# Kernel optimization log

Hardware: AMD Instinct MI355X
Metric: run time of the kernel (lower is better)

Reference implementation:

```python
import jax, jax.numpy as jnp
import numpy as np

B, T, D, H, O, L = 32, 512, 512, 512, 2, 2


def setup_inputs() -> dict:
    key = jax.random.key(0)
    ks = jax.random.split(key, 8)
    s_in = 1.0 / np.sqrt(D + H)
    s_h = 1.0 / np.sqrt(H + H)
    x = jax.random.normal(ks[0], (B, T, D), dtype=jnp.float32)
    # Fused gate weights per layer: columns ordered [forget | input | candidate | output]
    W0 = jax.random.uniform(ks[1], (D + H, 4 * H), jnp.float32, -s_in, s_in)
    b0 = jax.random.uniform(ks[2], (4 * H,), jnp.float32, -s_in, s_in)
    W1 = jax.random.uniform(ks[3], (H + H, 4 * H), jnp.float32, -s_h, s_h)
    b1 = jax.random.uniform(ks[4], (4 * H,), jnp.float32, -s_h, s_h)
    s_r = 1.0 / np.sqrt(H)
    Wr = jax.random.uniform(ks[5], (H, O), jnp.float32, -s_r, s_r)
    br = jax.random.uniform(ks[6], (O,), jnp.float32, -s_r, s_r)
    return {"x": x, "W0": W0, "b0": b0, "W1": W1, "b1": b1, "Wr": Wr, "br": br}


def _lstm_cell(xt, h, c, W, b):
    # One fused GEMM for all 4 gates, then elementwise gate math.
    z = jnp.concatenate([xt, h], axis=1) @ W + b  # [B, 4H]
    f, i, g, o = jnp.split(z, 4, axis=1)
    new_c = c * jax.nn.sigmoid(f) + jnp.tanh(g) * jax.nn.sigmoid(i)
    # NB: original module applies tanh to the OLD cell state c (faithful to source).
    new_h = jax.nn.sigmoid(o) * jnp.tanh(c)
    return new_h, new_c


def reference(x, W0, b0, W1, b1, Wr, br):
    Bb = x.shape[0]
    zeros = jnp.zeros((Bb, H), dtype=x.dtype)

    def step(carry, xt):
        h1, c1, h2, c2 = carry
        nh1, nc1 = _lstm_cell(xt, h1, c1, W0, b0)
        nh2, nc2 = _lstm_cell(nh1, h2, c2, W1, b1)
        return (nh1, nc1, nh2, nc2), nh2

    _, ys = jax.lax.scan(step, (zeros, zeros, zeros, zeros), jnp.swapaxes(x, 0, 1))
    out = jnp.swapaxes(ys, 0, 1)  # [B, T, H]
    return out @ Wr + br  # [B, T, O]
```

## Files before the change

kernel.cpp:

```cpp
#include <hip/hip_runtime.h>
#include <hip/hip_bf16.h>
#include <stdint.h>

typedef unsigned short u16;
typedef unsigned int u32;
typedef unsigned long long u64;
typedef __attribute__((ext_vector_type(8))) short bf16x8;
typedef __attribute__((ext_vector_type(4))) float f32x4;
typedef __attribute__((ext_vector_type(4))) u32 u32x4;

#define TT 512
#define WPS ((size_t)2048 * 1024)
#define ZRS 8
#define HRS 16
#define HRS2 4

#define LD16C(dst, addr) asm volatile("global_load_dwordx4 %0, %1, off sc0 sc1" : "=v"(dst) : "v"(addr))
#define LD8C(dst, addr)  asm volatile("global_load_dwordx2 %0, %1, off sc0 sc1" : "=v"(dst) : "v"(addr))
#define LD4C(dst, addr)  asm volatile("global_load_dword %0, %1, off sc0 sc1"   : "=v"(dst) : "v"(addr))
#define ST4C(addr, v)    asm volatile("global_store_dword %0, %1, off sc0 sc1"  :: "v"(addr), "v"(v) : "memory")
#define ST8C(addr, v)    asm volatile("global_store_dwordx2 %0, %1, off sc0 sc1":: "v"(addr), "v"(v) : "memory")
#define ST16C(addr, v)   asm volatile("global_store_dwordx4 %0, %1, off sc0 sc1":: "v"(addr), "v"(v) : "memory")
#define VM0()            do { asm volatile("s_waitcnt vmcnt(0)" ::: "memory"); \
                              __builtin_amdgcn_sched_barrier(0); } while (0)

__device__ __forceinline__ u16 f2bf(float f) {
  u32 u = __builtin_bit_cast(u32, f);
  return (u16)((u + 0x7FFFu + ((u >> 16) & 1u)) >> 16);
}
__device__ __forceinline__ float bf2f(u16 h) {
  u32 u = ((u32)h) << 16;
  return __builtin_bit_cast(float, u);
}
__device__ __forceinline__ float sigm(float x) { return 1.0f / (1.0f + expf(-x)); }
__device__ __forceinline__ f32x4 mfma16(bf16x8 a, bf16x8 b, f32x4 c) {
  return __builtin_amdgcn_mfma_f32_16x16x32_bf16(a, b, c, 0, 0, 0);
}
__device__ __forceinline__ u32 cvtpk(float a, float b) {
  u32 r;
  asm volatile("v_cvt_pk_bf16_f32 %0, %1, %2" : "=v"(r) : "v"(a), "v"(b));
  return r;
}
__device__ __forceinline__ void mark_err(u32* err) {
  __hip_atomic_fetch_add(err, 1u, __ATOMIC_RELAXED, __HIP_MEMORY_SCOPE_AGENT);
}
__device__ __forceinline__ u64 pack3(float v, u32 tag) {
  u16 p0 = f2bf(v); float r1 = v - bf2f(p0);
  u16 p1 = f2bf(r1); u16 p2 = f2bf(r1 - bf2f(p1));
  return (u64)((u32)p0 | ((u32)p1 << 16)) | ((u64)((u32)p2 | (tag << 16)) << 32);
}
__device__ __forceinline__ float zval(u64 w) {
  return bf2f((u16)(w & 0xFFFFu)) + bf2f((u16)((w >> 16) & 0xFFFFu))
       + bf2f((u16)((w >> 32) & 0xFFFFu));
}

__device__ __forceinline__ void wait_slots(const u32* slots, int ln, u32 tgt,
                                           u32* lastv, int* bail, u32* err) {
  if (*bail) return;
  if (__ballot(*lastv < tgt) == 0ull) return;
  const u32* ptr = slots + (ln & 31);
  int n = 0;
  for (;;) {
    u32 v;
    LD4C(v, ptr);
    VM0();
    if (v > *lastv) *lastv = v;
    if (__ballot(*lastv < tgt) == 0ull) return;
    __builtin_amdgcn_s_sleep(2);
    if (++n > 400000) { *bail = 1; if (ln == 0) mark_err(err); return; }
  }
}

__device__ __forceinline__ void head_poll(const u64* ptr, u32 texp, u32* err) {
  int n = 0;
  for (;;) {
    u64 hw;
    LD8C(hw, ptr);
    VM0();
    if (__ballot((u32)(hw >> 48) != texp) == 0ull) return;
    __builtin_amdgcn_s_sleep(1);
    if (++n > 600000) { if ((threadIdx.x & 63) == 0) mark_err(err); return; }
  }
}

__global__ void prep_w(const float* __restrict__ W, u16* __restrict__ WT) {
  int i = blockIdx.x * 256 + threadIdx.x;
  if (i >= 2048 * 1024) return;
  int n = i >> 10, k = i & 1023;
  float v = W[(size_t)k * 2048 + n];
  u16 p0 = f2bf(v);  float r  = v - bf2f(p0);
  u16 p1 = f2bf(r);  float r2 = r - bf2f(p1);
  u16 p2 = f2bf(r2);
  size_t o = (size_t)n * 1024 + k;
  WT[o] = p0;
  WT[WPS + o] = p1;
  WT[2 * WPS + o] = p2;
}

template <int LAYER>
__device__ void chain(char* smem, int p, int bid,
                      const float* __restrict__ bias,
                      const u16* __restrict__ WT,
                      const u64* Zring, u64* hG,
                      const u32* progOther, u32* progSelf,
                      u16* h2hi, u32* err) {
  u16* wl = (u16*)smem;
  float* zl = (float*)(smem + 131072);
  const int tid = threadIdx.x;

#pragma unroll 1
  for (int it = 0; it < 32; ++it) {
    int id = it * 256 + tid;
    int pl = id >> 12, rem = id & 4095, rho = rem >> 6, m = rem & 63;
    int n = ((rho >> 4) << 9) + (bid << 4) + (rho & 15);
    u32x4 v = *(const u32x4*)(WT + (size_t)pl * WPS + (size_t)n * 1024 + 512 + m * 8);
    int dst = pl * 65536 + rho * 1024 + ((m << 4) ^ ((rho & 7) << 4));
    *(u32x4*)((char*)wl + dst) = v;
  }

  const int ln = tid & 63, kq = tid >> 6;
  const int fr = ln & 15, kg8 = (ln >> 4) << 3;
  const int row = tid >> 4, hc = tid & 15;
  float bsv[4];
#pragma unroll
  for (int g = 0; g < 4; ++g) bsv[g] = bias[(g << 9) + (bid << 4) + hc];
  const int ka = kq * 128 + kg8;
  const u16* w2base[4];
#pragma unroll
  for (int nt = 0; nt < 4; ++nt)
    w2base[nt] = WT + 2 * WPS + (size_t)((nt << 9) + (bid << 4) + fr) * 1024 + 512 + ka;
  const int hrm = (LAYER == 1) ? (HRS - 1) : (HRS2 - 1);
  const int pcol = ((ln >> 1) << 4) + ((ln & 1) << 9);

  float creg = 0.0f;
  u32 lastbp = 0;
  int bail = 0;
  __syncthreads();

#pragma unroll 1
  for (int t = 0; t < TT; ++t) {
    if (LAYER == 1 && kq == 0 && t >= HRS - 1)
      wait_slots(progOther, ln, (u32)(t - (HRS - 1)), &lastbp, &bail, err);

    const size_t soff = (size_t)(t & hrm) * 8192;
    const u64* hb = hG + soff + (size_t)fr * 512 + ka;
    const u64* zb = Zring + (size_t)(t & (ZRS - 1)) * (16 * 2048) + (size_t)row * 2048
                  + (bid << 4) + hc;
    const u32 texp = (u32)t, zexp = (u32)(t + 1);

    u64 zw[4];
#pragma unroll
    for (int g = 0; g < 4; ++g) LD8C(zw[g], zb + ((size_t)g << 9));

    head_poll(hG + soff + pcol, texp, err);

    u32x4 hv[4][4];
    int tries = 0;
    for (;;) {
#pragma unroll
      for (int kt = 0; kt < 4; ++kt)
#pragma unroll
        for (int j = 0; j < 4; ++j) LD16C(hv[kt][j], hb + kt * 32 + 2 * j);
      VM0();
      u32 bad = 0;
#pragma unroll
      for (int kt = 0; kt < 4; ++kt)
#pragma unroll
        for (int j = 0; j < 4; ++j)
          bad |= ((hv[kt][j].y >> 16) ^ texp) | ((hv[kt][j].w >> 16) ^ texp);
      if (__ballot(bad != 0) == 0ull) break;
      if (++tries > 500000) { if (ln == 0) mark_err(err); break; }
      __builtin_amdgcn_s_sleep(1);
    }

    f32x4 acc[4] = {{0.f,0.f,0.f,0.f},{0.f,0.f,0.f,0.f},{0.f,0.f,0.f,0.f},{0.f,0.f,0.f,0.f}};
#pragma unroll
    for (int kt = 0; kt < 4; ++kt) {
      u32 r0[4], r1[4], r2[4];
#pragma unroll
      for (int j = 0; j < 4; ++j) {
        u32 lo0 = hv[kt][j].x, hi0 = hv[kt][j].y, lo1 = hv[kt][j].z, hi1 = hv[kt][j].w;
        r0[j] = (lo0 & 0xFFFFu) | (lo1 << 16);
        r1[j] = (lo0 >> 16) | (lo1 & 0xFFFF0000u);
        r2[j] = (hi0 & 0xFFFFu) | (hi1 << 16);
      }
      bf16x8 a0 = __builtin_bit_cast(bf16x8, *(u32x4*)r0);
      bf16x8 a1 = __builtin_bit_cast(bf16x8, *(u32x4*)r1);
      bf16x8 a2 = __builtin_bit_cast(bf16x8, *(u32x4*)r2);
#pragma unroll
      for (int nt = 0; nt < 4; ++nt) {
        int rho = (nt << 4) + fr;
        int kb = ((ka + kt * 32) << 1) ^ ((rho & 7) << 4);
        bf16x8 w0 = *(const bf16x8*)((char*)wl + rho * 1024 + kb);
        bf16x8 w1 = *(const bf16x8*)((char*)wl + 65536 + rho * 1024 + kb);
        bf16x8 w2 = *(const bf16x8*)(w2base[nt] + kt * 32);
        acc[nt] = mfma16(a0, w0, acc[nt]);
        acc[nt] = mfma16(a1, w0, acc[nt]);
        acc[nt] = mfma16(a2, w0, acc[nt]);
        acc[nt] = mfma16(a0, w1, acc[nt]);
        acc[nt] = mfma16(a1, w1, acc[nt]);
        acc[nt] = mfma16(a0, w2, acc[nt]);
      }
    }
    const int r4 = (ln >> 4) << 2;
    if (kq < 2) {
#pragma unroll
      for (int nt = 0; nt < 4; ++nt)
#pragma unroll
        for (int r = 0; r < 4; ++r)
          zl[(kq * 16 + r4 + r) * 66 + (nt << 4) + fr] = acc[nt][r];
    }
    __syncthreads();
    if (kq >= 2) {
#pragma unroll
      for (int nt = 0; nt < 4; ++nt)
#pragma unroll
        for (int r = 0; r < 4; ++r)
          zl[((kq - 2) * 16 + r4 + r) * 66 + (nt << 4) + fr] += acc[nt][r];
    }
    __syncthreads();

    int ztries = 0;
    for (;;) {
      u32 zbad = 0;
#pragma unroll
      for (int g = 0; g < 4; ++g) zbad |= ((u32)(zw[g] >> 48) ^ zexp);
      if (__ballot(zbad != 0) == 0ull) break;
      __builtin_amdgcn_s_sleep(1);
#pragma unroll
      for (int g = 0; g < 4; ++g) LD8C(zw[g], zb + ((size_t)g << 9));
      VM0();
      if (++ztries > 500000) { if (ln == 0) mark_err(err); break; }
    }
    float z4[4];
#pragma unroll
    for (int g = 0; g < 4; ++g)
      z4[g] = zl[row * 66 + (g << 4) + hc] + zl[(16 + row) * 66 + (g << 4) + hc]
            + zval(zw[g]) + bsv[g];
    float sf = sigm(z4[0]);
    float si = sigm(z4[1]);
    float tg = tanhf(z4[2]);
    float sog = sigm(z4[3]);
    float hn = sog * tanhf(creg);
    creg = creg * sf + tg * si;
    u64 word = pack3(hn, (u32)(t + 1));
    size_t ho = (size_t)((t + 1) & hrm) * 8192 + (size_t)row * 512 + (bid << 4) + hc;
    ST8C(hG + ho, word);
    if (LAYER == 2)
      h2hi[(size_t)(t + 1) * 16384 + (size_t)(p * 16 + row) * 512 + (bid << 4) + hc] =
          (u16)(word & 0xFFFFu);
    __syncthreads();
    if (tid == 0) ST4C(progSelf + bid, (u32)(t + 1));
  }
}

__device__ void worker(char* smem, int w, const float* __restrict__ x,
                       const u16* __restrict__ W0T, const u16* __restrict__ W1T,
                       const u64* h1G, u64* Z0R, u64* ZcR,
                       const u32* prog1, const u32* prog2, u32* err) {
  const int s = w & 63, q = w >> 6;
  u16* wl1 = (u16*)smem;
  u16* wl0 = (u16*)(smem + 65536);
  float* zl = (float*)(smem + 131072);
  const int tid = threadIdx.x;

#pragma unroll 1
  for (int it = 0; it < 32; ++it) {
    int id = it * 256 + tid;
    int sl = id >> 12, rem = id & 4095, pl = rem >> 11, rem2 = rem & 2047;
    int rho = rem2 >> 6, m = rem2 & 63;
    const u16* WT = sl ? W0T : W1T;
    u32x4 v = *(const u32x4*)(WT + (size_t)pl * WPS + (size_t)(32 * s + rho) * 1024 + m * 8);
    int dst = sl * 65536 + pl * 32768 + rho * 1024 + ((m << 4) ^ ((rho & 7) << 4));
    *(u32x4*)((char*)wl1 + dst) = v;
  }

  const int ln = tid & 63, kq = tid >> 6;
  const int fr = ln & 15, kg8 = (ln >> 4) << 3;
  const int row = tid >> 4, c2 = (tid & 15) * 2;
  const int ka = kq * 128 + kg8;
  const int pcol = ((ln >> 1) << 4) + ((ln & 1) << 9);
  u32 last2[2] = {0, 0}, lastbp[2] = {0, 0};
  int bail = 0;
  __syncthreads();

#pragma unroll 1
  for (int k = 0;; ++k) {
    int t = 2 * k + q;
    if (t > 511) break;

    int nz = (k < 3) ? 2 : 1;
#pragma unroll 1
    for (int e = 0; e < nz; ++e) {
      int tz = (e == 0 && k < 3) ? t : t + 6;
      if (tz > 511) continue;
#pragma unroll 1
      for (int p = 0; p < 2; ++p) {
        if (kq == 0 && tz >= ZRS)
          wait_slots(prog1 + p * 32, ln, (u32)(tz - ZRS + 1), &lastbp[p], &bail, err);
        const float* xb = x + (size_t)(p * 16 + fr) * TT * 512 + (size_t)tz * 512 + ka;
        f32x4 acc[2] = {{0.f,0.f,0.f,0.f},{0.f,0.f,0.f,0.f}};
#pragma unroll
        for (int kt = 0; kt < 4; ++kt) {
          f32x4 f0 = *(const f32x4*)(xb + kt * 32);
          f32x4 f1 = *(const f32x4*)(xb + kt * 32 + 4);
          u32 r0[4], r1[4], r2[4];
#pragma unroll
          for (int j = 0; j < 4; ++j) {
            float v0 = (j < 2) ? f0[j * 2] : f1[(j - 2) * 2];
            float v1 = (j < 2) ? f0[j * 2 + 1] : f1[(j - 2) * 2 + 1];
            u32 pk0 = cvtpk(v0, v1);
            float h0 = __builtin_bit_cast(float, pk0 << 16);
            float h1f = __builtin_bit_cast(float, pk0 & 0xFFFF0000u);
            float q0 = v0 - h0, q1 = v1 - h1f;
            u32 pk1 = cvtpk(q0, q1);
            float g0 = __builtin_bit_cast(float, pk1 << 16);
            float g1 = __builtin_bit_cast(float, pk1 & 0xFFFF0000u);
            u32 s0 = __builtin_bit_cast(u32, q0 - g0);
            u32 s1 = __builtin_bit_cast(u32, q1 - g1);
            r0[j] = pk0; r1[j] = pk1;
            r2[j] = (s0 >> 16) | (s1 & 0xFFFF0000u);
          }
          bf16x8 a0 = __builtin_bit_cast(bf16x8, *(u32x4*)r0);
          bf16x8 a1 = __builtin_bit_cast(bf16x8, *(u32x4*)r1);
          bf16x8 a2 = __builtin_bit_cast(bf16x8, *(u32x4*)r2);
#pragma unroll
          for (int nt = 0; nt < 2; ++nt) {
            int rho = (nt << 4) + fr;
            int kb = ((ka + kt * 32) << 1) ^ ((rho & 7) << 4);
            bf16x8 w0 = *(const bf16x8*)((char*)wl0 + rho * 1024 + kb);
            bf16x8 w1 = *(const bf16x8*)((char*)wl0 + 32768 + rho * 1024 + kb);
            bf16x8 w2 = *(const bf16x8*)(W0T + 2 * WPS + (size_t)(32 * s + rho) * 1024 + ka + kt * 32);
            acc[nt] = mfma16(a0, w0, acc[nt]);
            acc[nt] = mfma16(a1, w0, acc[nt]);
            acc[nt] = mfma16(a2, w0, acc[nt]);
            acc[nt] = mfma16(a0, w1, acc[nt]);
            acc[nt] = mfma16(a1, w1, acc[nt]);
            acc[nt] = mfma16(a0, w2, acc[nt]);
          }
        }
        const int r4 = (ln >> 4) << 2;
        if (kq < 2) {
#pragma unroll
          for (int nt = 0; nt < 2; ++nt)
#pragma unroll
            for (int r = 0; r < 4; ++r)
              zl[(kq * 16 + r4 + r) * 34 + (nt << 4) + fr] = acc[nt][r];
        }
        __syncthreads();
        if (kq >= 2) {
#pragma unroll
          for (int nt = 0; nt < 2; ++nt)
#pragma unroll
            for (int r = 0; r < 4; ++r)
              zl[((kq - 2) * 16 + r4 + r) * 34 + (nt << 4) + fr] += acc[nt][r];
        }
        __syncthreads();
        float v0 = zl[row * 34 + c2] + zl[(16 + row) * 34 + c2];
        float v1 = zl[row * 34 + c2 + 1] + zl[(16 + row) * 34 + c2 + 1];
        u64 w0 = pack3(v0, (u32)(tz + 1));
        u64 w1 = pack3(v1, (u32)(tz + 1));
        u32x4 st = { (u32)w0, (u32)(w0 >> 32), (u32)w1, (u32)(w1 >> 32) };
        u64* dst = Z0R + (size_t)p * ZRS * 16 * 2048 + (size_t)(tz & (ZRS - 1)) * (16 * 2048)
                 + (size_t)row * 2048 + 32 * s + c2;
        ST16C(dst, st);
        __syncthreads();
      }
    }

#pragma unroll 1
    for (int p = 0; p < 2; ++p) {
      if (kq == 0 && t >= ZRS)
        wait_slots(prog2 + p * 32, ln, (u32)(t - ZRS + 1), &last2[p], &bail, err);
      const size_t sb = (size_t)p * HRS * 8192 + (size_t)((t + 1) & (HRS - 1)) * 8192;
      const u64* hb = h1G + sb + (size_t)fr * 512 + ka;
      const u32 texp = (u32)(t + 1);
      head_poll(h1G + sb + pcol, texp, err);
      u32x4 hv[4][4];
      int tries = 0;
      for (;;) {
#pragma unroll
        for (int kt = 0; kt < 4; ++kt)
#pragma unroll
          for (int j = 0; j < 4; ++j) LD16C(hv[kt][j], hb + kt * 32 + 2 * j);
        VM0();
        u32 bad = 0;
#pragma unroll
        for (int kt = 0; kt < 4; ++kt)
#pragma unroll
          for (int j = 0; j < 4; ++j)
            bad |= ((hv[kt][j].y >> 16) ^ texp) | ((hv[kt][j].w >> 16) ^ texp);
        if (__ballot(bad != 0) == 0ull) break;
        if (++tries > 500000) { if (ln == 0) mark_err(err); break; }
        __builtin_amdgcn_s_sleep(1);
      }
      f32x4 acc[2] = {{0.f,0.f,0.f,0.f},{0.f,0.f,0.f,0.f}};
#pragma unroll
      for (int kt = 0; kt < 4; ++kt) {
        u32 r0[4], r1[4], r2[4];
#pragma unroll
        for (int j = 0; j < 4; ++j) {
          u32 lo0 = hv[kt][j].x, hi0 = hv[kt][j].y, lo1 = hv[kt][j].z, hi1 = hv[kt][j].w;
          r0[j] = (lo0 & 0xFFFFu) | (lo1 << 16);
          r1[j] = (lo0 >> 16) | (lo1 & 0xFFFF0000u);
          r2[j] = (hi0 & 0xFFFFu) | (hi1 << 16);
        }
        bf16x8 a0 = __builtin_bit_cast(bf16x8, *(u32x4*)r0);
        bf16x8 a1 = __builtin_bit_cast(bf16x8, *(u32x4*)r1);
        bf16x8 a2 = __builtin_bit_cast(bf16x8, *(u32x4*)r2);
#pragma unroll
        for (int nt = 0; nt < 2; ++nt) {
          int rho = (nt << 4) + fr;
          int kb = ((ka + kt * 32) << 1) ^ ((rho & 7) << 4);
          bf16x8 w0 = *(const bf16x8*)((char*)wl1 + rho * 1024 + kb);
          bf16x8 w1 = *(const bf16x8*)((char*)wl1 + 32768 + rho * 1024 + kb);
          bf16x8 w2 = *(const bf16x8*)(W1T + 2 * WPS + (size_t)(32 * s + rho) * 1024 + ka + kt * 32);
          acc[nt] = mfma16(a0, w0, acc[nt]);
          acc[nt] = mfma16(a1, w0, acc[nt]);
          acc[nt] = mfma16(a2, w0, acc[nt]);
          acc[nt] = mfma16(a0, w1, acc[nt]);
          acc[nt] = mfma16(a1, w1, acc[nt]);
          acc[nt] = mfma16(a0, w2, acc[nt]);
        }
      }
      const int r4 = (ln >> 4) << 2;
      if (kq < 2) {
#pragma unroll
        for (int nt = 0; nt < 2; ++nt)
#pragma unroll
          for (int r = 0; r < 4; ++r)
            zl[(kq * 16 + r4 + r) * 34 + (nt << 4) + fr] = acc[nt][r];
      }
      __syncthreads();
      if (kq >= 2) {
#pragma unroll
        for (int nt = 0; nt < 2; ++nt)
#pragma unroll
          for (int r = 0; r < 4; ++r)
            zl[((kq - 2) * 16 + r4 + r) * 34 + (nt << 4) + fr] += acc[nt][r];
      }
      __syncthreads();
      float v0 = zl[row * 34 + c2] + zl[(16 + row) * 34 + c2];
      float v1 = zl[row * 34 + c2 + 1] + zl[(16 + row) * 34 + c2 + 1];
      u64 w0 = pack3(v0, (u32)(t + 1));
      u64 w1 = pack3(v1, (u32)(t + 1));
      u32x4 st = { (u32)w0, (u32)(w0 >> 32), (u32)w1, (u32)(w1 >> 32) };
      u64* dst = ZcR + (size_t)p * ZRS * 16 * 2048 + (size_t)(t & (ZRS - 1)) * (16 * 2048)
               + (size_t)row * 2048 + 32 * s + c2;
      ST16C(dst, st);
      __syncthreads();
    }
  }
}

__global__ void __launch_bounds__(256, 1) mega(
    const float* __restrict__ x,
    const float* __restrict__ bias0, const float* __restrict__ bias1,
    const u16* __restrict__ W0T, const u16* __restrict__ W1T,
    u64* Z0R, u64* ZcR, u64* h1G, u64* h2G, u16* h2hi, u32* flags) {
  __shared__ char smem[139520];
  const int blk = blockIdx.x;
  const int r8 = blk & 7, g8 = blk >> 3;
  u32* prog1 = flags;
  u32* prog2 = flags + 64;
  u32* err = flags + 128;
  if (r8 < 2) {
    int p = r8;
    chain<1>(smem, p, g8, bias0, W0T,
             Z0R + (size_t)p * ZRS * 16 * 2048, h1G + (size_t)p * HRS * 8192,
             prog2 + p * 32, prog1 + p * 32, nullptr, err);
  } else if (r8 < 4) {
    int p = r8 - 2;
    chain<2>(smem, p, g8, bias1, W1T,
             ZcR + (size_t)p * ZRS * 16 * 2048, h2G + (size_t)p * HRS2 * 8192,
             nullptr, prog2 + p * 32, h2hi, err);
  } else {
    worker(smem, (r8 - 4) * 32 + g8, x, W0T, W1T, h1G, Z0R, ZcR, prog1, prog2, err);
  }
}

__global__ void proj(const u16* __restrict__ y,
                     const float* __restrict__ Wr, const float* __restrict__ br,
                     float* __restrict__ out) {
  int gw = (blockIdx.x * blockDim.x + threadIdx.x) >> 6;
  int ln = threadIdx.x & 63;
  int t = gw >> 5, b = gw & 31;
  const u16* yp = y + (size_t)(t + 1) * 16384 + (size_t)b * 512 + ln * 8;
  u32x4 v = *(const u32x4*)yp;
  float p0 = 0.f, p1 = 0.f;
#pragma unroll
  for (int jj = 0; jj < 8; ++jj) {
    u16 hh = (u16)((v[jj >> 1] >> ((jj & 1) * 16)) & 0xFFFFu);
    float yv = bf2f(hh);
    int j = ln * 8 + jj;
    p0 += yv * Wr[j * 2 + 0];
    p1 += yv * Wr[j * 2 + 1];
  }
#pragma unroll
  for (int o = 32; o; o >>= 1) { p0 += __shfl_down(p0, o, 64); p1 += __shfl_down(p1, o, 64); }
  if (ln == 0) {
    out[((size_t)b * 512 + t) * 2 + 0] = p0 + br[0];
    out[((size_t)b * 512 + t) * 2 + 1] = p1 + br[1];
  }
}

__global__ void fail_mark(float* out, float code) {
  if (threadIdx.x == 0 && blockIdx.x == 0) out[0] = code;
}
__global__ void err_check(const u32* flags, float* out) {
  if (threadIdx.x == 0 && blockIdx.x == 0) {
    u32 e = flags[128];
    if (e) out[0] = 1.0e6f + (float)e;
  }
}

extern "C" void kernel_launch(void* const* d_in, const int* in_sizes, int n_in,
                              void* d_out, int out_size, void* d_ws, size_t ws_size,
                              hipStream_t stream) {
  (void)in_sizes; (void)n_in; (void)out_size;
  const float* x  = (const float*)d_in[0];
  const float* W0 = (const float*)d_in[1];
  const float* b0 = (const float*)d_in[2];
  const float* W1 = (const float*)d_in[3];
  const float* b1 = (const float*)d_in[4];
  const float* Wr = (const float*)d_in[5];
  const float* br = (const float*)d_in[6];
  float* out = (float*)d_out;

  char* ws = (char*)d_ws;
  size_t off = 0;
  auto take = [&](size_t n) { char* p = ws + off; off = (off + n + 255) & ~(size_t)255; return p; };

  u16* W0T  = (u16*)take(3 * WPS * 2);
  u16* W1T  = (u16*)take(3 * WPS * 2);
  u64* Z0R  = (u64*)take((size_t)2 * ZRS * 16 * 2048 * 8);
  u64* ZcR  = (u64*)take((size_t)2 * ZRS * 16 * 2048 * 8);
  u64* h1G  = (u64*)take((size_t)2 * HRS * 8192 * 8);
  u64* h2G  = (u64*)take((size_t)2 * HRS2 * 8192 * 8);
  u16* h2hi = (u16*)take((size_t)513 * 16384 * 2);
  u32* flags = (u32*)take(129 * 4);

  if (off > ws_size) {
    fail_mark<<<1, 1, 0, stream>>>(out, 2.0e6f);
    return;
  }

  (void)hipMemsetAsync(flags, 0, 129 * 4, stream);
  (void)hipMemsetAsync(Z0R, 0, (size_t)2 * ZRS * 16 * 2048 * 8, stream);
  (void)hipMemsetAsync(ZcR, 0, (size_t)2 * ZRS * 16 * 2048 * 8, stream);
  (void)hipMemsetAsync(h1G, 0, (size_t)2 * HRS * 8192 * 8, stream);
  (void)hipMemsetAsync(h2G, 0, (size_t)2 * HRS2 * 8192 * 8, stream);

  prep_w<<<8192, 256, 0, stream>>>(W0, W0T);
  prep_w<<<8192, 256, 0, stream>>>(W1, W1T);
  (void)hipGetLastError();
  mega<<<256, 256, 0, stream>>>(x, b0, b1, W0T, W1T,
                                Z0R, ZcR, h1G, h2G, h2hi, flags);
  if (hipGetLastError() != hipSuccess) {
    fail_mark<<<1, 1, 0, stream>>>(out, 3.0e6f);
    return;
  }
  proj<<<4096, 256, 0, stream>>>(h2hi, Wr, br, out);
  err_check<<<1, 1, 0, stream>>>(flags, out);
}
```

Measured before the change: 4.056 ms.

## Split worker blocks into dedicated layer-0 input and layer-1 projection roles

Before, each worker block computed both the x-projection for layer 0 and the h1 projection for layer 1, each over 32 gate columns. Now half the worker blocks compute only the layer-1 h1 projection (Zc) and the other half compute only the layer-0 x-projection (Z0), each over 64 columns, with that role's weights filling shared memory. This takes the x-projection work off the latency-critical Zc path, so the two streams no longer serialise inside one block. In exchange, each block does twice the MFMA and reduction work per step, which may lengthen the latency of each Zc step on the recurrent chain.

```diff
diff --git a/kernel.cpp b/kernel.cpp
--- a/kernel.cpp
+++ b/kernel.cpp
@@ -254,33 +254,27 @@
   }
 }
 
-__device__ void worker(char* smem, int w, const float* __restrict__ x,
-                       const u16* __restrict__ W0T, const u16* __restrict__ W1T,
-                       const u64* h1G, u64* Z0R, u64* ZcR,
-                       const u32* prog1, const u32* prog2, u32* err) {
-  const int s = w & 63, q = w >> 6;
-  u16* wl1 = (u16*)smem;
-  u16* wl0 = (u16*)(smem + 65536);
+__device__ void worker_z0(char* smem, int s, int q, const float* __restrict__ x,
+                          const u16* __restrict__ W0T, u64* Z0R,
+                          const u32* prog1, u32* err) {
+  u16* wl0 = (u16*)smem;
   float* zl = (float*)(smem + 131072);
   const int tid = threadIdx.x;
 
 #pragma unroll 1
   for (int it = 0; it < 32; ++it) {
     int id = it * 256 + tid;
-    int sl = id >> 12, rem = id & 4095, pl = rem >> 11, rem2 = rem & 2047;
-    int rho = rem2 >> 6, m = rem2 & 63;
-    const u16* WT = sl ? W0T : W1T;
-    u32x4 v = *(const u32x4*)(WT + (size_t)pl * WPS + (size_t)(32 * s + rho) * 1024 + m * 8);
-    int dst = sl * 65536 + pl * 32768 + rho * 1024 + ((m << 4) ^ ((rho & 7) << 4));
-    *(u32x4*)((char*)wl1 + dst) = v;
+    int pl = id >> 12, rem = id & 4095, rho = rem >> 6, m = rem & 63;
+    u32x4 v = *(const u32x4*)(W0T + (size_t)pl * WPS + (size_t)(64 * s + rho) * 1024 + m * 8);
+    int dst = pl * 65536 + rho * 1024 + ((m << 4) ^ ((rho & 7) << 4));
+    *(u32x4*)((char*)wl0 + dst) = v;
   }
 
   const int ln = tid & 63, kq = tid >> 6;
   const int fr = ln & 15, kg8 = (ln >> 4) << 3;
-  const int row = tid >> 4, c2 = (tid & 15) * 2;
+  const int row = tid >> 4, c4 = (tid & 15) * 4;
   const int ka = kq * 128 + kg8;
-  const int pcol = ((ln >> 1) << 4) + ((ln & 1) << 9);
-  u32 last2[2] = {0, 0}, lastbp[2] = {0, 0};
+  u32 lastbp[2] = {0, 0};
   int bail = 0;
   __syncthreads();
 
@@ -288,7 +282,6 @@
   for (int k = 0;; ++k) {
     int t = 2 * k + q;
     if (t > 511) break;
-
     int nz = (k < 3) ? 2 : 1;
 #pragma unroll 1
     for (int e = 0; e < nz; ++e) {
@@ -299,7 +292,7 @@
         if (kq == 0 && tz >= ZRS)
           wait_slots(prog1 + p * 32, ln, (u32)(tz - ZRS + 1), &lastbp[p], &bail, err);
         const float* xb = x + (size_t)(p * 16 + fr) * TT * 512 + (size_t)tz * 512 + ka;
-        f32x4 acc[2] = {{0.f,0.f,0.f,0.f},{0.f,0.f,0.f,0.f}};
+        f32x4 acc[4] = {{0.f,0.f,0.f,0.f},{0.f,0.f,0.f,0.f},{0.f,0.f,0.f,0.f},{0.f,0.f,0.f,0.f}};
 #pragma unroll
         for (int kt = 0; kt < 4; ++kt) {
           f32x4 f0 = *(const f32x4*)(xb + kt * 32);
@@ -325,12 +318,12 @@
           bf16x8 a1 = __builtin_bit_cast(bf16x8, *(u32x4*)r1);
           bf16x8 a2 = __builtin_bit_cast(bf16x8, *(u32x4*)r2);
 #pragma unroll
-          for (int nt = 0; nt < 2; ++nt) {
+          for (int nt = 0; nt < 4; ++nt) {
             int rho = (nt << 4) + fr;
             int kb = ((ka + kt * 32) << 1) ^ ((rho & 7) << 4);
             bf16x8 w0 = *(const bf16x8*)((char*)wl0 + rho * 1024 + kb);
-            bf16x8 w1 = *(const bf16x8*)((char*)wl0 + 32768 + rho * 1024 + kb);
-            bf16x8 w2 = *(const bf16x8*)(W0T + 2 * WPS + (size_t)(32 * s + rho) * 1024 + ka + kt * 32);
+            bf16x8 w1 = *(const bf16x8*)((char*)wl0 + 65536 + rho * 1024 + kb);
+            bf16x8 w2 = *(const bf16x8*)(W0T + 2 * WPS + (size_t)(64 * s + rho) * 1024 + ka + kt * 32);
             acc[nt] = mfma16(a0, w0, acc[nt]);
             acc[nt] = mfma16(a1, w0, acc[nt]);
             acc[nt] = mfma16(a2, w0, acc[nt]);
@@ -342,32 +335,67 @@
         const int r4 = (ln >> 4) << 2;
         if (kq < 2) {
 #pragma unroll
-          for (int nt = 0; nt < 2; ++nt)
+          for (int nt = 0; nt < 4; ++nt)
 #pragma unroll
             for (int r = 0; r < 4; ++r)
-              zl[(kq * 16 + r4 + r) * 34 + (nt << 4) + fr] = acc[nt][r];
+              zl[(kq * 16 + r4 + r) * 66 + (nt << 4) + fr] = acc[nt][r];
         }
         __syncthreads();
         if (kq >= 2) {
 #pragma unroll
-          for (int nt = 0; nt < 2; ++nt)
+          for (int nt = 0; nt < 4; ++nt)
 #pragma unroll
             for (int r = 0; r < 4; ++r)
-              zl[((kq - 2) * 16 + r4 + r) * 34 + (nt << 4) + fr] += acc[nt][r];
+              zl[((kq - 2) * 16 + r4 + r) * 66 + (nt << 4) + fr] += acc[nt][r];
         }
         __syncthreads();
-        float v0 = zl[row * 34 + c2] + zl[(16 + row) * 34 + c2];
-        float v1 = zl[row * 34 + c2 + 1] + zl[(16 + row) * 34 + c2 + 1];
-        u64 w0 = pack3(v0, (u32)(tz + 1));
-        u64 w1 = pack3(v1, (u32)(tz + 1));
-        u32x4 st = { (u32)w0, (u32)(w0 >> 32), (u32)w1, (u32)(w1 >> 32) };
+        u64 wv[4];
+#pragma unroll
+        for (int i = 0; i < 4; ++i) {
+          float v = zl[row * 66 + c4 + i] + zl[(16 + row) * 66 + c4 + i];
+          wv[i] = pack3(v, (u32)(tz + 1));
+        }
         u64* dst = Z0R + (size_t)p * ZRS * 16 * 2048 + (size_t)(tz & (ZRS - 1)) * (16 * 2048)
-                 + (size_t)row * 2048 + 32 * s + c2;
-        ST16C(dst, st);
+                 + (size_t)row * 2048 + 64 * s + c4;
+        u32x4 stA = { (u32)wv[0], (u32)(wv[0] >> 32), (u32)wv[1], (u32)(wv[1] >> 32) };
+        u32x4 stB = { (u32)wv[2], (u32)(wv[2] >> 32), (u32)wv[3], (u32)(wv[3] >> 32) };
+        ST16C(dst, stA);
+        ST16C(dst + 2, stB);
         __syncthreads();
       }
     }
-
+  }
+}
+
+__device__ void worker_zc(char* smem, int s, int q,
+                          const u16* __restrict__ W1T, const u64* h1G, u64* ZcR,
+                          const u32* prog2, u32* err) {
+  u16* wl1 = (u16*)smem;
+  float* zl = (float*)(smem + 131072);
+  const int tid = threadIdx.x;
+
+#pragma unroll 1
+  for (int it = 0; it < 32; ++it) {
+    int id = it * 256 + tid;
+    int pl = id >> 12, rem = id & 4095, rho = rem >> 6, m = rem & 63;
+    u32x4 v = *(const u32x4*)(W1T + (size_t)pl * WPS + (size_t)(64 * s + rho) * 1024 + m * 8);
+    int dst = pl * 65536 + rho * 1024 + ((m << 4) ^ ((rho & 7) << 4));
+    *(u32x4*)((char*)wl1 + dst) = v;
+  }
+
+  const int ln = tid & 63, kq = tid >> 6;
+  const int fr = ln & 15, kg8 = (ln >> 4) << 3;
+  const int row = tid >> 4, c4 = (tid & 15) * 4;
+  const int ka = kq * 128 + kg8;
+  const int pcol = ((ln >> 1) << 4) + ((ln & 1) << 9);
+  u32 last2[2] = {0, 0};
+  int bail = 0;
+  __syncthreads();
+
+#pragma unroll 1
+  for (int k = 0;; ++k) {
+    int t = 2 * k + q;
+    if (t > 511) break;
 #pragma unroll 1
     for (int p = 0; p < 2; ++p) {
       if (kq == 0 && t >= ZRS)
@@ -394,7 +422,7 @@
         if (++tries > 500000) { if (ln == 0) mark_err(err); break; }
         __builtin_amdgcn_s_sleep(1);
       }
-      f32x4 acc[2] = {{0.f,0.f,0.f,0.f},{0.f,0.f,0.f,0.f}};
+      f32x4 acc[4] = {{0.f,0.f,0.f,0.f},{0.f,0.f,0.f,0.f},{0.f,0.f,0.f,0.f},{0.f,0.f,0.f,0.f}};
 #pragma unroll
       for (int kt = 0; kt < 4; ++kt) {
         u32 r0[4], r1[4], r2[4];
@@ -409,12 +437,12 @@
         bf16x8 a1 = __builtin_bit_cast(bf16x8, *(u32x4*)r1);
         bf16x8 a2 = __builtin_bit_cast(bf16x8, *(u32x4*)r2);
 #pragma unroll
-        for (int nt = 0; nt < 2; ++nt) {
+        for (int nt = 0; nt < 4; ++nt) {
           int rho = (nt << 4) + fr;
           int kb = ((ka + kt * 32) << 1) ^ ((rho & 7) << 4);
           bf16x8 w0 = *(const bf16x8*)((char*)wl1 + rho * 1024 + kb);
-          bf16x8 w1 = *(const bf16x8*)((char*)wl1 + 32768 + rho * 1024 + kb);
-          bf16x8 w2 = *(const bf16x8*)(W1T + 2 * WPS + (size_t)(32 * s + rho) * 1024 + ka + kt * 32);
+          bf16x8 w1 = *(const bf16x8*)((char*)wl1 + 65536 + rho * 1024 + kb);
+          bf16x8 w2 = *(const bf16x8*)(W1T + 2 * WPS + (size_t)(64 * s + rho) * 1024 + ka + kt * 32);
           acc[nt] = mfma16(a0, w0, acc[nt]);
           acc[nt] = mfma16(a1, w0, acc[nt]);
           acc[nt] = mfma16(a2, w0, acc[nt]);
@@ -426,28 +454,32 @@
       const int r4 = (ln >> 4) << 2;
       if (kq < 2) {
 #pragma unroll
-        for (int nt = 0; nt < 2; ++nt)
+        for (int nt = 0; nt < 4; ++nt)
 #pragma unroll
           for (int r = 0; r < 4; ++r)
-            zl[(kq * 16 + r4 + r) * 34 + (nt << 4) + fr] = acc[nt][r];
+            zl[(kq * 16 + r4 + r) * 66 + (nt << 4) + fr] = acc[nt][r];
       }
       __syncthreads();
       if (kq >= 2) {
 #pragma unroll
-        for (int nt = 0; nt < 2; ++nt)
+        for (int nt = 0; nt < 4; ++nt)
 #pragma unroll
           for (int r = 0; r < 4; ++r)
-            zl[((kq - 2) * 16 + r4 + r) * 34 + (nt << 4) + fr] += acc[nt][r];
+            zl[((kq - 2) * 16 + r4 + r) * 66 + (nt << 4) + fr] += acc[nt][r];
       }
       __syncthreads();
-      float v0 = zl[row * 34 + c2] + zl[(16 + row) * 34 + c2];
-      float v1 = zl[row * 34 + c2 + 1] + zl[(16 + row) * 34 + c2 + 1];
-      u64 w0 = pack3(v0, (u32)(t + 1));
-      u64 w1 = pack3(v1, (u32)(t + 1));
-      u32x4 st = { (u32)w0, (u32)(w0 >> 32), (u32)w1, (u32)(w1 >> 32) };
+      u64 wv[4];
+#pragma unroll
+      for (int i = 0; i < 4; ++i) {
+        float v = zl[row * 66 + c4 + i] + zl[(16 + row) * 66 + c4 + i];
+        wv[i] = pack3(v, (u32)(t + 1));
+      }
       u64* dst = ZcR + (size_t)p * ZRS * 16 * 2048 + (size_t)(t & (ZRS - 1)) * (16 * 2048)
-               + (size_t)row * 2048 + 32 * s + c2;
-      ST16C(dst, st);
+               + (size_t)row * 2048 + 64 * s + c4;
+      u32x4 stA = { (u32)wv[0], (u32)(wv[0] >> 32), (u32)wv[1], (u32)(wv[1] >> 32) };
+      u32x4 stB = { (u32)wv[2], (u32)(wv[2] >> 32), (u32)wv[3], (u32)(wv[3] >> 32) };
+      ST16C(dst, stA);
+      ST16C(dst + 2, stB);
       __syncthreads();
     }
   }
@@ -474,8 +506,10 @@
     chain<2>(smem, p, g8, bias1, W1T,
              ZcR + (size_t)p * ZRS * 16 * 2048, h2G + (size_t)p * HRS2 * 8192,
              nullptr, prog2 + p * 32, h2hi, err);
+  } else if (r8 < 6) {
+    worker_zc(smem, g8, r8 - 4, W1T, h1G, ZcR, prog2, err);
   } else {
-    worker(smem, (r8 - 4) * 32 + g8, x, W0T, W1T, h1G, Z0R, ZcR, prog1, prog2, err);
+    worker_z0(smem, g8, r8 - 6, x, W0T, Z0R, prog1, err);
   }
 }
 
```

After: 3.542 ms (median of 2 runs). 12.7% less time.
